# Optimization experiments

Hardware: AMD Instinct MI355X
Metric: run time of the kernel (lower is better)

The kernel has to match this reference:

```python
import jax, jax.numpy as jnp
import numpy as np

INPUT_DIM, HIDDEN, OUTPUT_DIM, NUM_LAYERS = 512, 128, 96, 5
BATCH, SEQ = 64, 512


def _gru_layer(x_seq, w_ih, w_hh, b_ih, b_hh):
    """Single GRU layer, PyTorch gate conventions. x_seq: [B,T,I] -> [B,T,H]."""
    B = x_seq.shape[0]
    H = w_hh.shape[1]
    # Precompute input-to-hidden gates for all timesteps: [B,T,3H]
    gx = jnp.einsum('bti,gi->btg', x_seq, w_ih) + b_ih

    def step(h, gx_t):
        gh = h @ w_hh.T + b_hh                      # [B,3H]
        xr, xz, xn = jnp.split(gx_t, 3, axis=-1)
        hr, hz, hn = jnp.split(gh, 3, axis=-1)
        r = jax.nn.sigmoid(xr + hr)
        z = jax.nn.sigmoid(xz + hz)
        n = jnp.tanh(xn + r * hn)
        h_new = (1.0 - z) * n + z * h
        return h_new, h_new

    h0 = jnp.zeros((B, H), x_seq.dtype)
    _, hs = jax.lax.scan(step, h0, jnp.swapaxes(gx, 0, 1))  # [T,B,H]
    return jnp.swapaxes(hs, 0, 1)                           # [B,T,H]


def setup_inputs() -> dict:
    key = jax.random.key(0)
    ks = jax.random.split(key, 8)
    s = 1.0 / np.sqrt(HIDDEN)  # torch default uniform init bound
    u = lambda k, shape: jax.random.uniform(k, shape, jnp.float32, -s, s)
    return {
        'x': jax.random.normal(ks[0], (BATCH, SEQ, INPUT_DIM), jnp.float32),
        'w_ih0': u(ks[1], (3 * HIDDEN, INPUT_DIM)),
        'w_ih_rest': u(ks[2], (NUM_LAYERS - 1, 3 * HIDDEN, HIDDEN)),
        'w_hh': u(ks[3], (NUM_LAYERS, 3 * HIDDEN, HIDDEN)),
        'b_ih': u(ks[4], (NUM_LAYERS, 3 * HIDDEN)),
        'b_hh': u(ks[5], (NUM_LAYERS, 3 * HIDDEN)),
        'fc_w': u(ks[6], (OUTPUT_DIM, HIDDEN)),
        'fc_b': u(ks[7], (OUTPUT_DIM,)),
    }


def reference(x, w_ih0, w_ih_rest, w_hh, b_ih, b_hh, fc_w, fc_b):
    h = _gru_layer(x, w_ih0, w_hh[0], b_ih[0], b_hh[0])
    for l in range(1, NUM_LAYERS):
        h = _gru_layer(h, w_ih_rest[l - 1], w_hh[l], b_ih[l], b_hh[l])
    # final linear on last timestep: [B,H] -> [B,OUTPUT_DIM]
    return h[:, -1, :] @ fc_w.T + fc_b
```

## Files before the change

kernel.cpp:

```cpp
#include <hip/hip_runtime.h>
#include <hip/hip_bf16.h>

#define BATCH   64
#define SEQ     512
#define IN0     512
#define HID     128
#define G3      384
#define NLAY    5
#define CHUNK   8

typedef _Float16 f16x8 __attribute__((ext_vector_type(8)));
typedef float    f32x4 __attribute__((ext_vector_type(4)));

static __device__ __forceinline__ float sigf(float x) {
    return __builtin_amdgcn_rcpf(1.f + __expf(-x));
}
static __device__ __forceinline__ float tanh_fast(float x) {
    const float e = __expf(-2.f * fabsf(x));
    return copysignf((1.f - e) * __builtin_amdgcn_rcpf(1.f + e), x);
}

__global__ __launch_bounds__(256) void gemm_gx(const float* __restrict__ A,
                                               const float* __restrict__ W,
                                               const float* __restrict__ bias,
                                               float* __restrict__ gx)
{
    __shared__ __align__(16) _Float16 As[64][40];
    __shared__ __align__(16) _Float16 Bs[64][40];

    const int tid  = threadIdx.x;
    const int lane = tid & 63;
    const int wv   = tid >> 6;
    const int n16  = lane & 15;
    const int quad = lane >> 4;
    const int row0 = blockIdx.x * 64;
    const int col0 = blockIdx.y * 64;
    const int r    = tid >> 2;
    const int kc   = (tid & 3) * 8;

    f32x4 acc[4];
    #pragma unroll
    for (int nt = 0; nt < 4; nt++) acc[nt] = (f32x4){0.f, 0.f, 0.f, 0.f};

    for (int k0 = 0; k0 < IN0; k0 += 32) {
        {
            const float* Ap = A + (size_t)(row0 + r) * IN0 + k0 + kc;
            float4 a0 = *(const float4*)(Ap);
            float4 a1 = *(const float4*)(Ap + 4);
            f16x8 v;
            v[0] = (_Float16)a0.x; v[1] = (_Float16)a0.y; v[2] = (_Float16)a0.z; v[3] = (_Float16)a0.w;
            v[4] = (_Float16)a1.x; v[5] = (_Float16)a1.y; v[6] = (_Float16)a1.z; v[7] = (_Float16)a1.w;
            *(f16x8*)&As[r][kc] = v;
        }
        {
            const float* Wp = W + (size_t)(col0 + r) * IN0 + k0 + kc;
            float4 b0 = *(const float4*)(Wp);
            float4 b1 = *(const float4*)(Wp + 4);
            f16x8 v;
            v[0] = (_Float16)b0.x; v[1] = (_Float16)b0.y; v[2] = (_Float16)b0.z; v[3] = (_Float16)b0.w;
            v[4] = (_Float16)b1.x; v[5] = (_Float16)b1.y; v[6] = (_Float16)b1.z; v[7] = (_Float16)b1.w;
            *(f16x8*)&Bs[r][kc] = v;
        }
        __syncthreads();

        const f16x8 af = *(const f16x8*)&As[wv * 16 + n16][quad * 8];
        #pragma unroll
        for (int nt = 0; nt < 4; nt++) {
            const f16x8 bfr = *(const f16x8*)&Bs[nt * 16 + n16][quad * 8];
            acc[nt] = __builtin_amdgcn_mfma_f32_16x16x32_f16(af, bfr, acc[nt], 0, 0, 0);
        }
        __syncthreads();
    }

    #pragma unroll
    for (int nt = 0; nt < 4; nt++) {
        const int col = col0 + nt * 16 + n16;
        const float bb = bias[col];
        #pragma unroll
        for (int r4 = 0; r4 < 4; r4++) {
            const int row = row0 + wv * 16 + quad * 4 + r4;
            gx[(size_t)row * G3 + col] = acc[nt][r4] + bb;
        }
    }
}

__global__ __launch_bounds__(512, 2) void gru_pipeline(
    const float* __restrict__ gx0,
    const float* __restrict__ w_ih_rest,
    const float* __restrict__ w_hh,
    const float* __restrict__ b_ih,
    const float* __restrict__ b_hh,
    _Float16* __restrict__ hmid,
    float* __restrict__ hlast,
    int* __restrict__ flags)
{
    const int l    = blockIdx.x >> 2;
    const int g    = blockIdx.x & 3;
    const int bm0  = g * 16;
    const int tid  = threadIdx.x;
    const int lane = tid & 63;
    const int n16  = lane & 15;
    const int quad = lane >> 4;
    const int wv   = tid >> 6;
    const int j    = wv * 16 + n16;

    __shared__ __align__(16) _Float16 hA[2][16][136];
    __shared__ int barcnt;

    f16x8 bf[3][4];
    {
        const float* wb = w_hh + (size_t)l * G3 * HID;
        #pragma unroll
        for (int tau = 0; tau < 3; tau++)
            #pragma unroll
            for (int kc = 0; kc < 4; kc++) {
                const float* wp = wb + (size_t)(tau * 128 + j) * HID + kc * 32 + quad * 8;
                f16x8 v;
                #pragma unroll
                for (int i = 0; i < 8; i++) v[i] = (_Float16)wp[i];
                bf[tau][kc] = v;
            }
    }
    f16x8 bi[3][4];
    if (l > 0) {
        const float* wb = w_ih_rest + (size_t)(l - 1) * G3 * HID;
        #pragma unroll
        for (int tau = 0; tau < 3; tau++)
            #pragma unroll
            for (int kc = 0; kc < 4; kc++) {
                const float* wp = wb + (size_t)(tau * 128 + j) * HID + kc * 32 + quad * 8;
                f16x8 v;
                #pragma unroll
                for (int i = 0; i < 8; i++) v[i] = (_Float16)wp[i];
                bi[tau][kc] = v;
            }
    }
    const float bcr = b_hh[l * G3 + j]       + ((l > 0) ? b_ih[l * G3 + j]       : 0.f);
    const float bcz = b_hh[l * G3 + j + 128] + ((l > 0) ? b_ih[l * G3 + j + 128] : 0.f);
    const float bcn = b_hh[l * G3 + j + 256];
    const float bxn = (l > 0) ? b_ih[l * G3 + j + 256] : 0.f;

    for (int i = tid; i < 2 * 16 * 136; i += 512) ((_Float16*)hA)[i] = (_Float16)0.f;
    float vhp[4] = {0.f, 0.f, 0.f, 0.f};
    if (tid == 0) barcnt = 0;

    const float* pR[4];
    float xr[4], xz[4], xn[4];
    if (l == 0) {
        #pragma unroll
        for (int r = 0; r < 4; r++) {
            pR[r] = gx0 + (size_t)(bm0 + quad * 4 + r) * SEQ * G3 + j;
            xr[r] = pR[r][0]; xz[r] = pR[r][128]; xn[r] = pR[r][256];
            pR[r] += G3;
        }
    }

    const _Float16* hprev = (l > 0) ? hmid + (size_t)((l - 1) * 4 + g) * SEQ * 2048 : (const _Float16*)nullptr;
    _Float16*       hpub  = (l < 4) ? hmid + (size_t)(l * 4 + g) * SEQ * 2048 : (_Float16*)nullptr;
    int*       dstflag = (l < 4) ? &flags[l * 4 + g] : (int*)nullptr;
    const int* srcflag = (l > 0) ? &flags[(l - 1) * 4 + g] : (const int*)nullptr;

    _Float16* hw = (l < 4) ? hpub + quad * 4 * 128 + j : (_Float16*)nullptr;

    f16x8 ap[4];
    const int hoff = n16 * 128 + quad * 8;

    __syncthreads();

    volatile int* bc = &barcnt;
    int btarget = 0;

    for (int c = 0; c < SEQ / CHUNK; c++) {
        const int t0 = c * CHUNK;

        if (l > 0) {
            const int need = t0 + CHUNK;
            int v = __hip_atomic_load(srcflag, __ATOMIC_RELAXED, __HIP_MEMORY_SCOPE_AGENT);
            while (v < need) {
                __builtin_amdgcn_s_sleep(2);
                v = __hip_atomic_load(srcflag, __ATOMIC_RELAXED, __HIP_MEMORY_SCOPE_AGENT);
            }
            (void)__hip_atomic_load(srcflag, __ATOMIC_ACQUIRE, __HIP_MEMORY_SCOPE_AGENT);
            __asm__ volatile("" ::: "memory");
            const _Float16* hp = hprev + (size_t)t0 * 2048 + hoff;
            #pragma unroll
            for (int kc = 0; kc < 4; kc++) ap[kc] = *(const f16x8*)(hp + kc * 32);
        }

        #pragma unroll
        for (int i = 0; i < CHUNK; i++) {
            const int t = t0 + i;

            __asm__ volatile("" ::: "memory");
            if (lane == 0) atomicAdd(&barcnt, 1);
            btarget += 8;
            while (*bc < btarget) { __builtin_amdgcn_s_sleep(1); }
            __asm__ volatile("" ::: "memory");

            const int buf = t & 1;
            f16x8 af[4];
            #pragma unroll
            for (int kc = 0; kc < 4; kc++)
                af[kc] = *(const f16x8*)&hA[buf][n16][kc * 32 + quad * 8];

            f32x4 ai0 = {0.f,0.f,0.f,0.f}, ai1 = ai0, ai2 = ai0;
            if (l > 0) {
                #pragma unroll
                for (int kc = 0; kc < 4; kc++) {
                    ai0 = __builtin_amdgcn_mfma_f32_16x16x32_f16(ap[kc], bi[0][kc], ai0, 0, 0, 0);
                    ai1 = __builtin_amdgcn_mfma_f32_16x16x32_f16(ap[kc], bi[1][kc], ai1, 0, 0, 0);
                    ai2 = __builtin_amdgcn_mfma_f32_16x16x32_f16(ap[kc], bi[2][kc], ai2, 0, 0, 0);
                }
            }
            float nr[4], nz[4], nn[4];
            if (l == 0) {
                #pragma unroll
                for (int r = 0; r < 4; r++) {
                    nr[r] = pR[r][0]; nz[r] = pR[r][128]; nn[r] = pR[r][256];
                }
                if (t + 1 < SEQ) {
                    #pragma unroll
                    for (int r = 0; r < 4; r++) pR[r] += G3;
                }
            }

            f32x4 ah0 = {0.f,0.f,0.f,0.f}, ah1 = ah0, ah2 = ah0;
            #pragma unroll
            for (int kc = 0; kc < 4; kc++) {
                ah0 = __builtin_amdgcn_mfma_f32_16x16x32_f16(af[kc], bf[0][kc], ah0, 0, 0, 0);
                ah1 = __builtin_amdgcn_mfma_f32_16x16x32_f16(af[kc], bf[1][kc], ah1, 0, 0, 0);
                ah2 = __builtin_amdgcn_mfma_f32_16x16x32_f16(af[kc], bf[2][kc], ah2, 0, 0, 0);
            }

            const int nbuf = buf ^ 1;
            #pragma unroll
            for (int r = 0; r < 4; r++) {
                const float sxr = (l == 0) ? xr[r] : ai0[r];
                const float sxz = (l == 0) ? xz[r] : ai1[r];
                const float sxn = ((l == 0) ? xn[r] : ai2[r]) + bxn;
                const float rg  = sigf(sxr + ah0[r] + bcr);
                const float zg  = sigf(sxz + ah1[r] + bcz);
                const float th  = tanh_fast(sxn + rg * (ah2[r] + bcn));
                const float hnew = fmaf(zg, vhp[r] - th, th);
                vhp[r] = hnew;
                hA[nbuf][quad * 4 + r][j] = (_Float16)hnew;
                if (l < 4) hw[r * 128] = (_Float16)hnew;
                if (l == 4 && t == SEQ - 1)
                    hlast[(bm0 + quad * 4 + r) * 128 + j] = hnew;
            }
            if (l < 4) hw += 2048;

            if (l == 0) {
                #pragma unroll
                for (int r = 0; r < 4; r++) { xr[r] = nr[r]; xz[r] = nz[r]; xn[r] = nn[r]; }
            }

            if (l > 0 && i < CHUNK - 1) {
                const _Float16* hp = hprev + (size_t)(t + 1) * 2048 + hoff;
                #pragma unroll
                for (int kc = 0; kc < 4; kc++) ap[kc] = *(const f16x8*)(hp + kc * 32);
            }
        }

        __syncthreads();
        if (l < 4 && tid == 0)
            __hip_atomic_store(dstflag, t0 + CHUNK, __ATOMIC_RELEASE, __HIP_MEMORY_SCOPE_AGENT);
    }
}

__global__ __launch_bounds__(128) void fc_kernel(const float* __restrict__ hlast,
                                                 const float* __restrict__ fc_w,
                                                 const float* __restrict__ fc_b,
                                                 float* __restrict__ out)
{
    const int b = blockIdx.x;
    const int o = threadIdx.x;
    if (o < 96) {
        const float* h = hlast + (size_t)b * HID;
        const float* wrow = fc_w + o * HID;
        float acc = fc_b[o];
        #pragma unroll 4
        for (int k = 0; k < HID; k++) acc = fmaf(h[k], wrow[k], acc);
        out[b * 96 + o] = acc;
    }
}

extern "C" void kernel_launch(void* const* d_in, const int* in_sizes, int n_in,
                              void* d_out, int out_size, void* d_ws, size_t ws_size,
                              hipStream_t stream)
{
    const float* x         = (const float*)d_in[0];
    const float* w_ih0     = (const float*)d_in[1];
    const float* w_ih_rest = (const float*)d_in[2];
    const float* w_hh      = (const float*)d_in[3];
    const float* b_ih      = (const float*)d_in[4];
    const float* b_hh      = (const float*)d_in[5];
    const float* fc_w      = (const float*)d_in[6];
    const float* fc_b      = (const float*)d_in[7];
    float* out = (float*)d_out;

    int*      flags = (int*)d_ws;
    float*    gxbuf = (float*)((char*)d_ws + 256);
    _Float16* hmid  = (_Float16*)((char*)d_ws + 256 + 50331648);
    float*    hlast = (float*)((char*)d_ws + 256 + 50331648 + 33554432);

    hipMemsetAsync(d_ws, 0, 256, stream);

    const dim3 gemmGrid(512, 6);
    gemm_gx<<<gemmGrid, 256, 0, stream>>>(x, w_ih0, b_ih, gxbuf);

    gru_pipeline<<<NLAY * 4, 512, 0, stream>>>(gxbuf, w_ih_rest, w_hh, b_ih, b_hh,
                                               hmid, hlast, flags);

    fc_kernel<<<BATCH, 128, 0, stream>>>(hlast, fc_w, fc_b, out);
}
```

Before: 986.0 us.

## Replace LDS atomic spin barrier with s_barrier and split MFMA accumulation chains

The per-timestep workgroup barrier, previously an LDS atomic counter with a sleep-spin loop, becomes a hardware s_barrier preceded by an explicit lgkmcnt wait and sched_barrier fences. The recurrent and input MFMA chains are also split into two independent accumulators per gate, summed at the end, to shorten the dependent MFMA latency chain on the serial critical path. The cost is more accumulator registers and a few extra vector adds, and correctness now depends on the manual waitcnt ordering the LDS writes before the barrier.

```diff
diff --git a/kernel.cpp b/kernel.cpp
--- a/kernel.cpp
+++ b/kernel.cpp
@@ -105,7 +105,6 @@
     const int j    = wv * 16 + n16;
 
     __shared__ __align__(16) _Float16 hA[2][16][136];
-    __shared__ int barcnt;
 
     f16x8 bf[3][4];
     {
@@ -142,7 +141,6 @@
 
     for (int i = tid; i < 2 * 16 * 136; i += 512) ((_Float16*)hA)[i] = (_Float16)0.f;
     float vhp[4] = {0.f, 0.f, 0.f, 0.f};
-    if (tid == 0) barcnt = 0;
 
     const float* pR[4];
     float xr[4], xz[4], xn[4];
@@ -166,9 +164,6 @@
     const int hoff = n16 * 128 + quad * 8;
 
     __syncthreads();
-
-    volatile int* bc = &barcnt;
-    int btarget = 0;
 
     for (int c = 0; c < SEQ / CHUNK; c++) {
         const int t0 = c * CHUNK;
@@ -191,11 +186,10 @@
         for (int i = 0; i < CHUNK; i++) {
             const int t = t0 + i;
 
-            __asm__ volatile("" ::: "memory");
-            if (lane == 0) atomicAdd(&barcnt, 1);
-            btarget += 8;
-            while (*bc < btarget) { __builtin_amdgcn_s_sleep(1); }
-            __asm__ volatile("" ::: "memory");
+            __builtin_amdgcn_sched_barrier(0);
+            __asm__ volatile("s_waitcnt lgkmcnt(0)" ::: "memory");
+            __builtin_amdgcn_s_barrier();
+            __builtin_amdgcn_sched_barrier(0);
 
             const int buf = t & 1;
             f16x8 af[4];
@@ -203,13 +197,18 @@
             for (int kc = 0; kc < 4; kc++)
                 af[kc] = *(const f16x8*)&hA[buf][n16][kc * 32 + quad * 8];
 
-            f32x4 ai0 = {0.f,0.f,0.f,0.f}, ai1 = ai0, ai2 = ai0;
+            const f32x4 z4 = {0.f, 0.f, 0.f, 0.f};
+            f32x4 ai0a = z4, ai1a = z4, ai2a = z4;
+            f32x4 ai0b = z4, ai1b = z4, ai2b = z4;
             if (l > 0) {
                 #pragma unroll
-                for (int kc = 0; kc < 4; kc++) {
-                    ai0 = __builtin_amdgcn_mfma_f32_16x16x32_f16(ap[kc], bi[0][kc], ai0, 0, 0, 0);
-                    ai1 = __builtin_amdgcn_mfma_f32_16x16x32_f16(ap[kc], bi[1][kc], ai1, 0, 0, 0);
-                    ai2 = __builtin_amdgcn_mfma_f32_16x16x32_f16(ap[kc], bi[2][kc], ai2, 0, 0, 0);
+                for (int kc = 0; kc < 2; kc++) {
+                    ai0a = __builtin_amdgcn_mfma_f32_16x16x32_f16(ap[kc],     bi[0][kc],     ai0a, 0, 0, 0);
+                    ai1a = __builtin_amdgcn_mfma_f32_16x16x32_f16(ap[kc],     bi[1][kc],     ai1a, 0, 0, 0);
+                    ai2a = __builtin_amdgcn_mfma_f32_16x16x32_f16(ap[kc],     bi[2][kc],     ai2a, 0, 0, 0);
+                    ai0b = __builtin_amdgcn_mfma_f32_16x16x32_f16(ap[kc + 2], bi[0][kc + 2], ai0b, 0, 0, 0);
+                    ai1b = __builtin_amdgcn_mfma_f32_16x16x32_f16(ap[kc + 2], bi[1][kc + 2], ai1b, 0, 0, 0);
+                    ai2b = __builtin_amdgcn_mfma_f32_16x16x32_f16(ap[kc + 2], bi[2][kc + 2], ai2b, 0, 0, 0);
                 }
             }
             float nr[4], nz[4], nn[4];
@@ -224,13 +223,23 @@
                 }
             }
 
-            f32x4 ah0 = {0.f,0.f,0.f,0.f}, ah1 = ah0, ah2 = ah0;
-            #pragma unroll
-            for (int kc = 0; kc < 4; kc++) {
-                ah0 = __builtin_amdgcn_mfma_f32_16x16x32_f16(af[kc], bf[0][kc], ah0, 0, 0, 0);
-                ah1 = __builtin_amdgcn_mfma_f32_16x16x32_f16(af[kc], bf[1][kc], ah1, 0, 0, 0);
-                ah2 = __builtin_amdgcn_mfma_f32_16x16x32_f16(af[kc], bf[2][kc], ah2, 0, 0, 0);
-            }
+            f32x4 ah0a = z4, ah1a = z4, ah2a = z4;
+            f32x4 ah0b = z4, ah1b = z4, ah2b = z4;
+            #pragma unroll
+            for (int kc = 0; kc < 2; kc++) {
+                ah0a = __builtin_amdgcn_mfma_f32_16x16x32_f16(af[kc],     bf[0][kc],     ah0a, 0, 0, 0);
+                ah1a = __builtin_amdgcn_mfma_f32_16x16x32_f16(af[kc],     bf[1][kc],     ah1a, 0, 0, 0);
+                ah2a = __builtin_amdgcn_mfma_f32_16x16x32_f16(af[kc],     bf[2][kc],     ah2a, 0, 0, 0);
+                ah0b = __builtin_amdgcn_mfma_f32_16x16x32_f16(af[kc + 2], bf[0][kc + 2], ah0b, 0, 0, 0);
+                ah1b = __builtin_amdgcn_mfma_f32_16x16x32_f16(af[kc + 2], bf[1][kc + 2], ah1b, 0, 0, 0);
+                ah2b = __builtin_amdgcn_mfma_f32_16x16x32_f16(af[kc + 2], bf[2][kc + 2], ah2b, 0, 0, 0);
+            }
+            const f32x4 ah0 = ah0a + ah0b;
+            const f32x4 ah1 = ah1a + ah1b;
+            const f32x4 ah2 = ah2a + ah2b;
+            const f32x4 ai0 = ai0a + ai0b;
+            const f32x4 ai1 = ai1a + ai1b;
+            const f32x4 ai2 = ai2a + ai2b;
 
             const int nbuf = buf ^ 1;
             #pragma unroll
```

After: 1.025 ms. +3.9%, slower.
